# Kernel tuning notes

Hardware: AMD Instinct MI355X
Metric: run time of the kernel (lower is better)

The kernel has to match this reference:

```python
import jax, jax.numpy as jnp
import numpy as np
from jax import lax

VOCAB, EMB, HID, SEQ, BATCH = 50000, 512, 256, 64, 128


def _lstm_dir(x, Wih, Whh, bih, bhh):
    # x: (L,B,E); Wih: (4H,E); Whh: (4H,H); torch gate order i,f,g,o
    B = x.shape[1]
    H = Whh.shape[1]
    xg = jnp.einsum('lbe,ge->lbg', x, Wih) + (bih + bhh)  # precompute input contribution

    def step(carry, g_in):
        h, c = carry
        g = g_in + h @ Whh.T
        i, f, gg, o = jnp.split(g, 4, axis=-1)
        c = jax.nn.sigmoid(f) * c + jax.nn.sigmoid(i) * jnp.tanh(gg)
        h = jax.nn.sigmoid(o) * jnp.tanh(c)
        return (h, c), h

    z = jnp.zeros((B, H), x.dtype)
    _, hs = lax.scan(step, (z, z), xg)
    return hs  # (L,B,H)


def _bilstm(x, Wih_f, Whh_f, bih_f, bhh_f, Wih_b, Whh_b, bih_b, bhh_b):
    hf = _lstm_dir(x, Wih_f, Whh_f, bih_f, bhh_f)
    hb = _lstm_dir(x[::-1], Wih_b, Whh_b, bih_b, bhh_b)[::-1]
    return jnp.concatenate([hf, hb], axis=-1)  # (L,B,2H)


def _forward(tokens1, tokens2, emb, Wih_f, Whh_f, bih_f, bhh_f, Wih_b, Whh_b, bih_b, bhh_b):
    L, B = tokens1.shape
    w = (Wih_f, Whh_f, bih_f, bhh_f, Wih_b, Whh_b, bih_b, bhh_b)
    # original applies self.lstm_1 to BOTH sentences (lstm_2 unused)
    o1 = _bilstm(emb[tokens1], *w)  # (L,B,D)
    o2 = _bilstm(emb[tokens2], *w)
    D = o1.shape[-1]
    mp1 = o1.max(axis=0)  # adaptive_max_pool1d over time -> (B,D)
    # torch .view on contiguous (L,B,D): raw reshape, replicated faithfully
    att = jnp.einsum('bd,bdl->bl', mp1, o2.reshape(B, D, L))
    att_sm = jax.nn.softmax(att, axis=1)  # per-row softmax over L
    new_pool = jnp.einsum('bl,bld->bd', att_sm, o2.reshape(B, L, D))
    # commonWords: d[i] = LAST index j in sen1 with sen1[j]==sen2[i], else -1
    s1, s2 = tokens1.T, tokens2.T  # (B,L)
    match = s2[:, :, None] == s1[:, None, :]  # (B,L2,L1)
    d = jnp.max(jnp.where(match, jnp.arange(L)[None, None, :], -1), axis=2)  # (B,L)
    mask = (d > 1) & (s2 > 0)  # note strict > 1 as in original
    pos = jnp.clip(d, 0, L - 1)
    o1b = jnp.transpose(o1, (1, 0, 2))  # (B,L,D)
    gath1 = jnp.take_along_axis(o1b, pos[:, :, None], axis=1)  # outputs_1[d[i], b]
    neg = jnp.finfo(o1.dtype).min
    has = jnp.any(mask, axis=1)[:, None]
    e1h = jnp.where(has, jnp.max(jnp.where(mask[:, :, None], gath1, neg), axis=1), 0.0)
    o2b = jnp.transpose(o2, (1, 0, 2))
    e2h = jnp.where(has, jnp.max(jnp.where(mask[:, :, None], o2b, neg), axis=1), 0.0)
    sim = jnp.exp(-jnp.sum(jnp.abs(mp1 - new_pool), axis=1))
    return sim, e1h, e2h


def setup_inputs() -> dict:
    key = jax.random.key(0)
    ks = jax.random.split(key, 8)
    H4 = 4 * HID

    def w(k, shape, fan):
        return (jax.random.normal(k, shape, jnp.float32) / np.float32(np.sqrt(fan))).astype(jnp.float32)

    return {
        'tokens1': jax.random.randint(ks[0], (SEQ, BATCH), 0, VOCAB),
        'tokens2': jax.random.randint(ks[1], (SEQ, BATCH), 0, VOCAB),
        'emb': jax.random.normal(ks[2], (VOCAB, EMB), jnp.float32) * 0.1,
        'Wih_f': w(ks[3], (H4, EMB), EMB),
        'Whh_f': w(ks[4], (H4, HID), HID),
        'bih_f': jnp.full((H4,), 0.01, jnp.float32),
        'bhh_f': jnp.full((H4,), 0.01, jnp.float32),
        'Wih_b': w(ks[5], (H4, EMB), EMB),
        'Whh_b': w(ks[6], (H4, HID), HID),
        'bih_b': jnp.full((H4,), 0.01, jnp.float32),
        'bhh_b': jnp.full((H4,), 0.01, jnp.float32),
    }


def reference(tokens1, tokens2, emb, Wih_f, Whh_f, bih_f, bhh_f, Wih_b, Whh_b, bih_b, bhh_b):
    return _forward(tokens1, tokens2, emb, Wih_f, Whh_f, bih_f, bhh_f, Wih_b, Whh_b, bih_b, bhh_b)
```

## Files before the change

### kernel.cpp

```cpp
#include <hip/hip_runtime.h>
#include <hip/hip_bf16.h>
#include <math.h>

#define L_SEQ 64
#define NB    128
#define EMBD  512
#define HID   256
#define G4    1024
#define NCOL  2048
#define DDIM  512
#define MS    (L_SEQ*NB)
#define MTOT  (2*MS)

typedef __bf16 bf16_t;
typedef bf16_t bf16x4 __attribute__((ext_vector_type(4)));
typedef bf16_t bf16x8 __attribute__((ext_vector_type(8)));
typedef float  floatx4 __attribute__((ext_vector_type(4)));
typedef float  floatx8 __attribute__((ext_vector_type(8)));

__device__ __forceinline__ bf16x8 cvt_bf16x8(floatx8 v) {
    bf16x8 r;
    r[0]=(bf16_t)v[0]; r[1]=(bf16_t)v[1]; r[2]=(bf16_t)v[2]; r[3]=(bf16_t)v[3];
    r[4]=(bf16_t)v[4]; r[5]=(bf16_t)v[5]; r[6]=(bf16_t)v[6]; r[7]=(bf16_t)v[7];
    return r;
}

__device__ __forceinline__ void gload_lds16(const bf16_t* g, bf16_t* l) {
    __builtin_amdgcn_global_load_lds(
        (const __attribute__((address_space(1))) unsigned int*)(g),
        (__attribute__((address_space(3))) unsigned int*)(l), 16, 0, 0);
}

__device__ __forceinline__ float fsigmoid(float x) {
    return __builtin_amdgcn_rcpf(1.0f + __expf(-x));
}
__device__ __forceinline__ float ftanh(float x) {
    return 1.0f - 2.0f * __builtin_amdgcn_rcpf(__expf(2.0f*x) + 1.0f);
}

#define LDS_BARRIER() asm volatile("s_waitcnt lgkmcnt(0)\n\ts_barrier" ::: "memory")

__global__ __launch_bounds__(256) void k_pack_a(const int* __restrict__ t1,
                                                const int* __restrict__ t2,
                                                const float* __restrict__ emb,
                                                bf16_t* __restrict__ A)
{
    int gid = blockIdx.x*256 + threadIdx.x;
    int row = gid >> 6;
    int k8  = (gid & 63) * 8;
    int tok = (row < MS) ? t1[row] : t2[row - MS];
    floatx8 v = *(const floatx8*)(emb + (size_t)tok*EMBD + k8);
    *(bf16x8*)(A + (size_t)row*EMBD + k8) = cvt_bf16x8(v);
}

__global__ __launch_bounds__(256) void k_pack_b(const float* __restrict__ wih_f,
                                                const float* __restrict__ wih_b,
                                                bf16_t* __restrict__ B)
{
    int gid = blockIdx.x*256 + threadIdx.x;
    int n   = gid >> 6;
    int k8  = (gid & 63) * 8;
    const float* src = (n >= 1024) ? (wih_b + (size_t)(n-1024)*EMBD)
                                   : (wih_f + (size_t)n*EMBD);
    *(bf16x8*)(B + (size_t)n*EMBD + k8) = cvt_bf16x8(*(const floatx8*)(src + k8));
}

__global__ __launch_bounds__(256) void k_pack_whh(const float* __restrict__ whh_f,
                                                  const float* __restrict__ whh_b,
                                                  bf16_t* __restrict__ whhB)
{
    int gid = blockIdx.x*256 + threadIdx.x;
    int r2  = gid >> 5;
    int k8  = (gid & 31) * 8;
    const float* src = (r2 >= 1024) ? (whh_b + (size_t)(r2-1024)*HID)
                                    : (whh_f + (size_t)r2*HID);
    *(bf16x8*)(whhB + (size_t)r2*HID + k8) = cvt_bf16x8(*(const floatx8*)(src + k8));
}

__global__ __launch_bounds__(256) void k_pack_bias(const float* __restrict__ bih_f,
                                                   const float* __restrict__ bhh_f,
                                                   const float* __restrict__ bih_b,
                                                   const float* __restrict__ bhh_b,
                                                   float* __restrict__ bias)
{
    int n = blockIdx.x*256 + threadIdx.x;
    bias[n] = (n >= 1024) ? (bih_b[n-1024] + bhh_b[n-1024])
                          : (bih_f[n] + bhh_f[n]);
}

__global__ __launch_bounds__(256) void xg_gemm4(const bf16_t* __restrict__ A,
                                                const bf16_t* __restrict__ B,
                                                const float* __restrict__ bias,
                                                bf16_t* __restrict__ xgT)
{
    __shared__ bf16_t As[128*32];
    __shared__ bf16_t Bs[128*32];
    const int tid  = threadIdx.x;
    const int wid  = tid >> 6;
    const int lane = tid & 63;
    const int l15  = lane & 15;
    const int quad = lane >> 4;
    const int m0   = blockIdx.y * 128;
    const int n0   = blockIdx.x * 128;
    const int mw   = (wid & 1) * 64;
    const int nw   = (wid >> 1) * 64;

    float biasv[4];
#pragma unroll
    for (int ni = 0; ni < 4; ++ni) biasv[ni] = bias[n0 + nw + ni*16 + l15];

    const int srow = tid >> 2;
    const int sk8  = (tid & 3) * 8;

    floatx4 acc[4][4] = {};
    for (int kk = 0; kk < EMBD; kk += 32) {
#pragma unroll
        for (int inst = 0; inst < 2; ++inst) {
            gload_lds16(A + (size_t)(m0 + inst*64 + srow)*EMBD + kk + sk8,
                        As + inst*2048 + wid*512);
            gload_lds16(B + (size_t)(n0 + inst*64 + srow)*EMBD + kk + sk8,
                        Bs + inst*2048 + wid*512);
        }
        __syncthreads();
        bf16x8 a[4], b[4];
#pragma unroll
        for (int mi = 0; mi < 4; ++mi)
            a[mi] = *(const bf16x8*)(As + (mw + mi*16 + l15)*32 + quad*8);
#pragma unroll
        for (int ni = 0; ni < 4; ++ni)
            b[ni] = *(const bf16x8*)(Bs + (nw + ni*16 + l15)*32 + quad*8);
#pragma unroll
        for (int mi = 0; mi < 4; ++mi)
#pragma unroll
            for (int ni = 0; ni < 4; ++ni)
                acc[mi][ni] = __builtin_amdgcn_mfma_f32_16x16x32_bf16(
                                  a[mi], b[ni], acc[mi][ni], 0, 0, 0);
        __syncthreads();
    }

    const int sent = blockIdx.y >> 6;
    const int l    = blockIdx.y & 63;
    const int dir  = n0 >> 10;
    const int s2   = sent*2 + dir;
#pragma unroll
    for (int mi = 0; mi < 4; ++mi)
#pragma unroll
        for (int ni = 0; ni < 4; ++ni) {
            int gcol = (n0 & 1023) + nw + ni*16 + l15;
            int b    = mw + mi*16 + quad*4;
            int ch   = b >> 4;
            int bi   = b & 15;
            bf16x4 v;
#pragma unroll
            for (int r = 0; r < 4; ++r) v[r] = (bf16_t)(acc[mi][ni][r] + biasv[ni]);
            *(bf16x4*)(xgT + ((size_t)((s2*8 + ch)*64 + l)*1024 + gcol)*16 + bi) = v;
        }
}

__global__
__attribute__((amdgpu_flat_work_group_size(512, 512), amdgpu_waves_per_eu(2, 2)))
void lstm_scan7(
    const bf16_t* __restrict__ whhB,
    const bf16_t* __restrict__ xgT,
    float* __restrict__ o1, float* __restrict__ o2)
{
    extern __shared__ char smem[];
    bf16_t* hb = (bf16_t*)smem;
    bf16_t* BL = (bf16_t*)(smem + 16384);

    const int tid  = threadIdx.x;
    const int wv   = tid >> 6;
    const int lane = tid & 63;
    const int l15  = lane & 15;
    const int quad = lane >> 4;
    const int s2   = blockIdx.y;
    const int sent = s2 >> 1;
    const int dr   = s2 & 1;
    const int chunk= blockIdx.x;
    const int b0   = chunk * 16;
    float* o = sent ? o2 : o1;
    const bf16_t* bb = whhB + (size_t)dr * (1024*HID);

#pragma unroll
    for (int nt = 0; nt < 8; ++nt) {
        const int g = nt >> 1, u = nt & 1;
        const int col = g*256 + wv*32 + u*16 + l15;
#pragma unroll
        for (int ksl = 0; ksl < 2; ++ksl)
            gload_lds16(bb + (size_t)col*HID + (4+ksl)*32 + quad*8,
                        BL + (size_t)(wv*16 + nt*2 + ksl)*512);
    }

    bf16x8 bwc[8][4];
#pragma unroll
    for (int nt = 0; nt < 8; ++nt) {
        const int g = nt >> 1, u = nt & 1;
        const bf16_t* cp = bb + (size_t)(g*256 + wv*32 + u*16 + l15)*HID + quad*8;
#pragma unroll
        for (int ks = 0; ks < 4; ++ks)
            bwc[nt][ks] = *(const volatile bf16x8*)(cp + ks*32);
    }

    for (int i = tid; i < 4096; i += 512) hb[i] = (bf16_t)0.0f;
    __syncthreads();

    float cst[2][4] = {};
    int pp = 0;

    bf16x4 xvc[8], xvn[8];
    {
        const int lt0 = dr ? (L_SEQ-1) : 0;
        const bf16_t* xp = xgT + (size_t)((s2*8 + chunk)*64 + lt0)*16384;
#pragma unroll
        for (int nt = 0; nt < 8; ++nt) {
            const int g = nt >> 1, u = nt & 1;
            xvc[nt] = *(const bf16x4*)(xp + (size_t)(g*256 + wv*32 + u*16 + l15)*16
                                       + quad*4);
        }
    }

    for (int t = 0; t < L_SEQ; ++t) {
        const int lt = dr ? (L_SEQ-1-t) : t;
        asm volatile("" ::: "memory");

        {
            const int tn  = (t < L_SEQ-1) ? t+1 : t;
            const int ltn = dr ? (L_SEQ-1-tn) : tn;
            const bf16_t* xp = xgT + (size_t)((s2*8 + chunk)*64 + ltn)*16384;
#pragma unroll
            for (int nt = 0; nt < 8; ++nt) {
                const int g = nt >> 1, u = nt & 1;
                xvn[nt] = *(const bf16x4*)(xp + (size_t)(g*256 + wv*32 + u*16 + l15)*16
                                           + quad*4);
            }
        }

        floatx4 acc[8] = {};
        if (t > 0) {
            bf16x8 sb6[8], sb7[8];
#pragma unroll
            for (int nt = 0; nt < 8; ++nt) {
                const int g = nt >> 1, u = nt & 1;
                const bf16_t* cp = bb + (size_t)(g*256 + wv*32 + u*16 + l15)*HID;
                sb6[nt] = *(const bf16x8*)(cp + 6*32 + quad*8);
                sb7[nt] = *(const bf16x8*)(cp + 7*32 + quad*8);
            }

            const bf16_t* fr = hb + pp*4096;
#pragma unroll
            for (int ks = 0; ks < 4; ++ks) {
                bf16x8 af = *(const bf16x8*)(fr + ((ks*4 + quad)*16 + l15)*8);
#pragma unroll
                for (int nt = 0; nt < 8; ++nt)
                    acc[nt] = __builtin_amdgcn_mfma_f32_16x16x32_bf16(
                                  af, bwc[nt][ks], acc[nt], 0, 0, 0);
            }
#pragma unroll
            for (int ksl = 0; ksl < 2; ++ksl) {
                bf16x8 af = *(const bf16x8*)(fr + (((4+ksl)*4 + quad)*16 + l15)*8);
#pragma unroll
                for (int nt = 0; nt < 8; ++nt) {
                    bf16x8 bl = *(const bf16x8*)(BL + (size_t)(wv*16 + nt*2 + ksl)*512
                                                 + lane*8);
                    acc[nt] = __builtin_amdgcn_mfma_f32_16x16x32_bf16(
                                  af, bl, acc[nt], 0, 0, 0);
                }
            }
            {
                bf16x8 af6 = *(const bf16x8*)(fr + ((6*4 + quad)*16 + l15)*8);
#pragma unroll
                for (int nt = 0; nt < 8; ++nt)
                    acc[nt] = __builtin_amdgcn_mfma_f32_16x16x32_bf16(
                                  af6, sb6[nt], acc[nt], 0, 0, 0);
                bf16x8 af7 = *(const bf16x8*)(fr + ((7*4 + quad)*16 + l15)*8);
#pragma unroll
                for (int nt = 0; nt < 8; ++nt)
                    acc[nt] = __builtin_amdgcn_mfma_f32_16x16x32_bf16(
                                  af7, sb7[nt], acc[nt], 0, 0, 0);
            }
        }

        bf16_t* fw = hb + (pp^1)*4096;
#pragma unroll
        for (int u = 0; u < 2; ++u) {
            const int j = wv*32 + u*16 + l15;
            float* orow = o + (size_t)(lt*NB + b0)*DDIM + dr*HID + j;
#pragma unroll
            for (int r = 0; r < 4; ++r) {
                const int m = quad*4 + r;
                float gi = acc[0*2+u][r] + (float)xvc[0*2+u][r];
                float gf = acc[1*2+u][r] + (float)xvc[1*2+u][r];
                float gg = acc[2*2+u][r] + (float)xvc[2*2+u][r];
                float go = acc[3*2+u][r] + (float)xvc[3*2+u][r];
                float cv = fsigmoid(gf)*cst[u][r] + fsigmoid(gi)*ftanh(gg);
                cst[u][r] = cv;
                float hv = fsigmoid(go)*ftanh(cv);
                orow[(size_t)m*DDIM] = hv;
                fw[((j >> 3)*16 + m)*8 + (j & 7)] = (bf16_t)hv;
            }
        }
#pragma unroll
        for (int nt = 0; nt < 8; ++nt) xvc[nt] = xvn[nt];
        LDS_BARRIER();
        pp ^= 1;
    }
}

__global__ __launch_bounds__(256) void k_mp1(const float* __restrict__ o1,
                                             float* __restrict__ mp1)
{
    int gid = blockIdx.x*256 + threadIdx.x;
    float m = -3.402823466e+38f;
    for (int l = 0; l < L_SEQ; ++l)
        m = fmaxf(m, o1[(size_t)l*(NB*DDIM) + gid]);
    mp1[gid] = m;
}

__global__ __launch_bounds__(256) void k_att(const float* __restrict__ o2,
                                             const float* __restrict__ mp1,
                                             float* __restrict__ sim)
{
    const int b   = blockIdx.x;
    const int tid = threadIdx.x;
    const int l   = tid & 63;
    const int cp  = tid >> 6;
    __shared__ float spart[256];
    __shared__ float satt[64], sexp[64], ssm[64];
    __shared__ float red[256];

    const float* o2b = o2  + (size_t)b*32768;
    const float* mpb = mp1 + b*DDIM;

    float p = 0.0f;
    for (int d = cp*128; d < cp*128 + 128; ++d)
        p += mpb[d] * o2b[d*64 + l];
    spart[tid] = p;
    __syncthreads();
    if (tid < 64)
        satt[tid] = spart[tid] + spart[tid+64] + spart[tid+128] + spart[tid+192];
    __syncthreads();
    if (tid < 64) {
        float mx = satt[0];
        for (int i = 1; i < 64; ++i) mx = fmaxf(mx, satt[i]);
        sexp[tid] = expf(satt[tid] - mx);
    }
    __syncthreads();
    if (tid < 64) {
        float s = 0.0f;
        for (int i = 0; i < 64; ++i) s += sexp[i];
        ssm[tid] = sexp[tid] / s;
    }
    __syncthreads();

    float np0 = 0.0f, np1 = 0.0f;
    for (int l2 = 0; l2 < 64; ++l2) {
        float smv = ssm[l2];
        np0 += smv * o2b[l2*DDIM + tid];
        np1 += smv * o2b[l2*DDIM + tid + 256];
    }
    float diff = fabsf(mpb[tid] - np0) + fabsf(mpb[tid+256] - np1);
    red[tid] = diff;
    __syncthreads();
    for (int s = 128; s > 0; s >>= 1) {
        if (tid < s) red[tid] += red[tid + s];
        __syncthreads();
    }
    if (tid == 0) sim[b] = expf(-red[0]);
}

__global__ __launch_bounds__(256) void k_common(
    const int*   __restrict__ t1, const int* __restrict__ t2,
    const float* __restrict__ o1, const float* __restrict__ o2,
    float* __restrict__ e1h, float* __restrict__ e2h)
{
    const int b   = blockIdx.x;
    const int tid = threadIdx.x;
    __shared__ int ss1[64];
    __shared__ int smask[64];
    __shared__ int spos[64];
    __shared__ int sany;
    if (tid == 0) sany = 0;
    if (tid < 64) ss1[tid] = t1[tid*NB + b];
    __syncthreads();
    if (tid < 64) {
        int s2 = t2[tid*NB + b];
        int dmax = -1;
        for (int j = 0; j < 64; ++j)
            if (ss1[j] == s2) dmax = j;
        int mk = (dmax > 1) && (s2 > 0);
        smask[tid] = mk;
        spos[tid]  = dmax < 0 ? 0 : dmax;
        if (mk) sany = 1;
    }
    __syncthreads();
    int has = sany;
#pragma unroll
    for (int half = 0; half < 2; ++half) {
        int dd = tid + half*256;
        float m1 = -3.402823466e+38f, m2 = -3.402823466e+38f;
        for (int i = 0; i < 64; ++i) {
            if (smask[i]) {
                m1 = fmaxf(m1, o1[(size_t)spos[i]*(NB*DDIM) + b*DDIM + dd]);
                m2 = fmaxf(m2, o2[(size_t)i      *(NB*DDIM) + b*DDIM + dd]);
            }
        }
        e1h[b*DDIM + dd] = has ? m1 : 0.0f;
        e2h[b*DDIM + dd] = has ? m2 : 0.0f;
    }
}

extern "C" void kernel_launch(void* const* d_in, const int* in_sizes, int n_in,
                              void* d_out, int out_size, void* d_ws, size_t ws_size,
                              hipStream_t stream)
{
    (void)in_sizes; (void)n_in; (void)out_size; (void)ws_size;
    const int*   t1    = (const int*)d_in[0];
    const int*   t2    = (const int*)d_in[1];
    const float* emb   = (const float*)d_in[2];
    const float* wih_f = (const float*)d_in[3];
    const float* whh_f = (const float*)d_in[4];
    const float* bih_f = (const float*)d_in[5];
    const float* bhh_f = (const float*)d_in[6];
    const float* wih_b = (const float*)d_in[7];
    const float* whh_b = (const float*)d_in[8];
    const float* bih_b = (const float*)d_in[9];
    const float* bhh_b = (const float*)d_in[10];
    float* out = (float*)d_out;

    char* ws = (char*)d_ws;
    size_t off = 0;
    auto carve = [&](size_t bytes) -> void* {
        void* p = ws + off;
        off = (off + bytes + 255) & ~(size_t)255;
        return p;
    };
    float*  o1    = (float*)carve(sizeof(float)*(size_t)L_SEQ*NB*DDIM);
    float*  o2    = (float*)carve(sizeof(float)*(size_t)L_SEQ*NB*DDIM);
    bf16_t* whhB  = (bf16_t*)carve(sizeof(bf16_t)*2*1024*HID);
    bf16_t* Bw    = (bf16_t*)carve(sizeof(bf16_t)*(size_t)NCOL*EMBD);
    float*  bias  = (float*)carve(sizeof(float)*NCOL);
    float*  mp1   = (float*)carve(sizeof(float)*NB*DDIM);
    bf16_t* xgT   = (bf16_t*)carve(sizeof(bf16_t)*(size_t)MTOT*NCOL);
    bf16_t* A     = (bf16_t*)o1;

    hipFuncSetAttribute((const void*)lstm_scan7,
                        hipFuncAttributeMaxDynamicSharedMemorySize, 147456);

    hipLaunchKernelGGL(k_pack_a,    dim3(4096), dim3(256), 0, stream, t1, t2, emb, A);
    hipLaunchKernelGGL(k_pack_b,    dim3(512),  dim3(256), 0, stream, wih_f, wih_b, Bw);
    hipLaunchKernelGGL(k_pack_whh,  dim3(256),  dim3(256), 0, stream, whh_f, whh_b, whhB);
    hipLaunchKernelGGL(k_pack_bias, dim3(8),    dim3(256), 0, stream,
                       bih_f, bhh_f, bih_b, bhh_b, bias);

    hipLaunchKernelGGL(xg_gemm4, dim3(16, 128), dim3(256), 0, stream, A, Bw, bias, xgT);

    hipLaunchKernelGGL(lstm_scan7, dim3(8, 4), dim3(512), 147456, stream,
                       whhB, xgT, o1, o2);

    hipLaunchKernelGGL(k_mp1,    dim3(256), dim3(256), 0, stream, o1, mp1);
    hipLaunchKernelGGL(k_att,    dim3(128), dim3(256), 0, stream, o2, mp1, out);
    hipLaunchKernelGGL(k_common, dim3(128), dim3(256), 0, stream,
                       t1, t2, o1, o2, out + NB, out + NB + NB*DDIM);
}
```

Before: 642.4 us.

## Split LSTM scan across 16 waves with one column tile per wave

The recurrent scan kernel now launches 1024 threads (16 waves) per block instead of 512, and each wave owns 16 hidden units across the four gates rather than 32. Per-wave register state (weight fragments, accumulators, cell state) is halved, which allows four waves per EU and more latency hiding on each serial timestep. The register double-buffered prefetch of the next step's input-gate values is dropped in favour of a load inside the step, and the k-slice 6/7 weight loads now share one staged register buffer. In exchange the block-wide barrier at every step now synchronises twice as many waves, and the input-gate load latency sits on the critical path.

```diff
diff --git a/kernel.cpp b/kernel.cpp
--- a/kernel.cpp
+++ b/kernel.cpp
@@ -158,8 +158,8 @@
 }
 
 __global__
-__attribute__((amdgpu_flat_work_group_size(512, 512), amdgpu_waves_per_eu(2, 2)))
-void lstm_scan7(
+__attribute__((amdgpu_flat_work_group_size(1024, 1024), amdgpu_waves_per_eu(4, 4)))
+void lstm_scan8(
     const bf16_t* __restrict__ whhB,
     const bf16_t* __restrict__ xgT,
     float* __restrict__ o1, float* __restrict__ o2)
@@ -181,69 +181,51 @@
     float* o = sent ? o2 : o1;
     const bf16_t* bb = whhB + (size_t)dr * (1024*HID);
 
-#pragma unroll
-    for (int nt = 0; nt < 8; ++nt) {
-        const int g = nt >> 1, u = nt & 1;
-        const int col = g*256 + wv*32 + u*16 + l15;
+
+#pragma unroll
+    for (int g = 0; g < 4; ++g) {
+        const int col = g*256 + wv*16 + l15;
 #pragma unroll
         for (int ksl = 0; ksl < 2; ++ksl)
             gload_lds16(bb + (size_t)col*HID + (4+ksl)*32 + quad*8,
-                        BL + (size_t)(wv*16 + nt*2 + ksl)*512);
-    }
-
-    bf16x8 bwc[8][4];
-#pragma unroll
-    for (int nt = 0; nt < 8; ++nt) {
-        const int g = nt >> 1, u = nt & 1;
-        const bf16_t* cp = bb + (size_t)(g*256 + wv*32 + u*16 + l15)*HID + quad*8;
+                        BL + (size_t)((wv*4 + g)*2 + ksl)*512);
+    }
+
+    bf16x8 bwc[4][4];
+#pragma unroll
+    for (int g = 0; g < 4; ++g) {
+        const bf16_t* cp = bb + (size_t)(g*256 + wv*16 + l15)*HID + quad*8;
 #pragma unroll
         for (int ks = 0; ks < 4; ++ks)
-            bwc[nt][ks] = *(const volatile bf16x8*)(cp + ks*32);
-    }
-
-    for (int i = tid; i < 4096; i += 512) hb[i] = (bf16_t)0.0f;
-    __syncthreads();
-
-    float cst[2][4] = {};
+            bwc[g][ks] = *(const volatile bf16x8*)(cp + ks*32);
+    }
+
+    for (int i = tid; i < 4096; i += 1024) hb[i] = (bf16_t)0.0f;
+    __syncthreads();
+
+    float cst[4] = {};
     int pp = 0;
-
-    bf16x4 xvc[8], xvn[8];
-    {
-        const int lt0 = dr ? (L_SEQ-1) : 0;
-        const bf16_t* xp = xgT + (size_t)((s2*8 + chunk)*64 + lt0)*16384;
-#pragma unroll
-        for (int nt = 0; nt < 8; ++nt) {
-            const int g = nt >> 1, u = nt & 1;
-            xvc[nt] = *(const bf16x4*)(xp + (size_t)(g*256 + wv*32 + u*16 + l15)*16
-                                       + quad*4);
-        }
-    }
 
     for (int t = 0; t < L_SEQ; ++t) {
         const int lt = dr ? (L_SEQ-1-t) : t;
         asm volatile("" ::: "memory");
 
+        bf16x4 xvc[4];
         {
-            const int tn  = (t < L_SEQ-1) ? t+1 : t;
-            const int ltn = dr ? (L_SEQ-1-tn) : tn;
-            const bf16_t* xp = xgT + (size_t)((s2*8 + chunk)*64 + ltn)*16384;
-#pragma unroll
-            for (int nt = 0; nt < 8; ++nt) {
-                const int g = nt >> 1, u = nt & 1;
-                xvn[nt] = *(const bf16x4*)(xp + (size_t)(g*256 + wv*32 + u*16 + l15)*16
-                                           + quad*4);
-            }
-        }
-
-        floatx4 acc[8] = {};
+            const bf16_t* xp = xgT + (size_t)((s2*8 + chunk)*64 + lt)*16384;
+#pragma unroll
+            for (int g = 0; g < 4; ++g)
+                xvc[g] = *(const bf16x4*)(xp + (size_t)(g*256 + wv*16 + l15)*16
+                                          + quad*4);
+        }
+
+        floatx4 acc[4] = {};
         if (t > 0) {
-            bf16x8 sb6[8], sb7[8];
-#pragma unroll
-            for (int nt = 0; nt < 8; ++nt) {
-                const int g = nt >> 1, u = nt & 1;
-                const bf16_t* cp = bb + (size_t)(g*256 + wv*32 + u*16 + l15)*HID;
-                sb6[nt] = *(const bf16x8*)(cp + 6*32 + quad*8);
-                sb7[nt] = *(const bf16x8*)(cp + 7*32 + quad*8);
+            bf16x8 sb[4];
+#pragma unroll
+            for (int g = 0; g < 4; ++g) {
+                const bf16_t* cp = bb + (size_t)(g*256 + wv*16 + l15)*HID;
+                sb[g] = *(const bf16x8*)(cp + 6*32 + quad*8);
             }
 
             const bf16_t* fr = hb + pp*4096;
@@ -251,56 +233,58 @@
             for (int ks = 0; ks < 4; ++ks) {
                 bf16x8 af = *(const bf16x8*)(fr + ((ks*4 + quad)*16 + l15)*8);
 #pragma unroll
-                for (int nt = 0; nt < 8; ++nt)
-                    acc[nt] = __builtin_amdgcn_mfma_f32_16x16x32_bf16(
-                                  af, bwc[nt][ks], acc[nt], 0, 0, 0);
+                for (int g = 0; g < 4; ++g)
+                    acc[g] = __builtin_amdgcn_mfma_f32_16x16x32_bf16(
+                                 af, bwc[g][ks], acc[g], 0, 0, 0);
+            }
+            {
+                bf16x8 af6 = *(const bf16x8*)(fr + ((6*4 + quad)*16 + l15)*8);
+#pragma unroll
+                for (int g = 0; g < 4; ++g)
+                    acc[g] = __builtin_amdgcn_mfma_f32_16x16x32_bf16(
+                                 af6, sb[g], acc[g], 0, 0, 0);
+            }
+#pragma unroll
+            for (int g = 0; g < 4; ++g) {
+                const bf16_t* cp = bb + (size_t)(g*256 + wv*16 + l15)*HID;
+                sb[g] = *(const bf16x8*)(cp + 7*32 + quad*8);
             }
 #pragma unroll
             for (int ksl = 0; ksl < 2; ++ksl) {
                 bf16x8 af = *(const bf16x8*)(fr + (((4+ksl)*4 + quad)*16 + l15)*8);
 #pragma unroll
-                for (int nt = 0; nt < 8; ++nt) {
-                    bf16x8 bl = *(const bf16x8*)(BL + (size_t)(wv*16 + nt*2 + ksl)*512
+                for (int g = 0; g < 4; ++g) {
+                    bf16x8 bl = *(const bf16x8*)(BL + (size_t)((wv*4 + g)*2 + ksl)*512
                                                  + lane*8);
-                    acc[nt] = __builtin_amdgcn_mfma_f32_16x16x32_bf16(
-                                  af, bl, acc[nt], 0, 0, 0);
+                    acc[g] = __builtin_amdgcn_mfma_f32_16x16x32_bf16(
+                                 af, bl, acc[g], 0, 0, 0);
                 }
             }
             {
-                bf16x8 af6 = *(const bf16x8*)(fr + ((6*4 + quad)*16 + l15)*8);
-#pragma unroll
-                for (int nt = 0; nt < 8; ++nt)
-                    acc[nt] = __builtin_amdgcn_mfma_f32_16x16x32_bf16(
-                                  af6, sb6[nt], acc[nt], 0, 0, 0);
                 bf16x8 af7 = *(const bf16x8*)(fr + ((7*4 + quad)*16 + l15)*8);
 #pragma unroll
-                for (int nt = 0; nt < 8; ++nt)
-                    acc[nt] = __builtin_amdgcn_mfma_f32_16x16x32_bf16(
-                                  af7, sb7[nt], acc[nt], 0, 0, 0);
+                for (int g = 0; g < 4; ++g)
+                    acc[g] = __builtin_amdgcn_mfma_f32_16x16x32_bf16(
+                                 af7, sb[g], acc[g], 0, 0, 0);
             }
         }
 
         bf16_t* fw = hb + (pp^1)*4096;
-#pragma unroll
-        for (int u = 0; u < 2; ++u) {
-            const int j = wv*32 + u*16 + l15;
-            float* orow = o + (size_t)(lt*NB + b0)*DDIM + dr*HID + j;
-#pragma unroll
-            for (int r = 0; r < 4; ++r) {
-                const int m = quad*4 + r;
-                float gi = acc[0*2+u][r] + (float)xvc[0*2+u][r];
-                float gf = acc[1*2+u][r] + (float)xvc[1*2+u][r];
-                float gg = acc[2*2+u][r] + (float)xvc[2*2+u][r];
-                float go = acc[3*2+u][r] + (float)xvc[3*2+u][r];
-                float cv = fsigmoid(gf)*cst[u][r] + fsigmoid(gi)*ftanh(gg);
-                cst[u][r] = cv;
-                float hv = fsigmoid(go)*ftanh(cv);
-                orow[(size_t)m*DDIM] = hv;
-                fw[((j >> 3)*16 + m)*8 + (j & 7)] = (bf16_t)hv;
-            }
-        }
-#pragma unroll
-        for (int nt = 0; nt < 8; ++nt) xvc[nt] = xvn[nt];
+        const int j = wv*16 + l15;
+        float* orow = o + (size_t)(lt*NB + b0)*DDIM + dr*HID + j;
+#pragma unroll
+        for (int r = 0; r < 4; ++r) {
+            const int m = quad*4 + r;
+            float gi = acc[0][r] + (float)xvc[0][r];
+            float gf = acc[1][r] + (float)xvc[1][r];
+            float gg = acc[2][r] + (float)xvc[2][r];
+            float go = acc[3][r] + (float)xvc[3][r];
+            float cv = fsigmoid(gf)*cst[r] + fsigmoid(gi)*ftanh(gg);
+            cst[r] = cv;
+            float hv = fsigmoid(go)*ftanh(cv);
+            orow[(size_t)m*DDIM] = hv;
+            fw[((j >> 3)*16 + m)*8 + (j & 7)] = (bf16_t)hv;
+        }
         LDS_BARRIER();
         pp ^= 1;
     }
@@ -443,7 +427,7 @@
     bf16_t* xgT   = (bf16_t*)carve(sizeof(bf16_t)*(size_t)MTOT*NCOL);
     bf16_t* A     = (bf16_t*)o1;
 
-    hipFuncSetAttribute((const void*)lstm_scan7,
+    hipFuncSetAttribute((const void*)lstm_scan8,
                         hipFuncAttributeMaxDynamicSharedMemorySize, 147456);
 
     hipLaunchKernelGGL(k_pack_a,    dim3(4096), dim3(256), 0, stream, t1, t2, emb, A);
@@ -454,7 +438,7 @@
 
     hipLaunchKernelGGL(xg_gemm4, dim3(16, 128), dim3(256), 0, stream, A, Bw, bias, xgT);
 
-    hipLaunchKernelGGL(lstm_scan7, dim3(8, 4), dim3(512), 147456, stream,
+    hipLaunchKernelGGL(lstm_scan8, dim3(8, 4), dim3(1024), 147456, stream,
                        whhB, xgT, o1, o2);
 
     hipLaunchKernelGGL(k_mp1,    dim3(256), dim3(256), 0, stream, o1, mp1);
```

New measurement: 618.4 us. -3.7%, faster.
